# Kernel optimization log

Hardware: AMD Instinct MI355X
Metric: run time of the kernel (lower is better)

## Reference

```python
import jax, jax.numpy as jnp
import numpy as np

MARGIN = 5.0  # margin_between_clusters


def setup_inputs() -> dict:
    key = jax.random.key(0)
    k1, k2, k3 = jax.random.split(key, 3)
    N, D, K = 262144, 128, 64
    embeddings = jax.random.normal(k1, (N, D), dtype=jnp.float32)
    cluster_labels = jax.random.randint(k2, (N,), 0, K, dtype=jnp.int64)
    centroids = jax.random.normal(k3, (K, D), dtype=jnp.float32)
    return {"embeddings": embeddings, "cluster_labels": cluster_labels, "centroids": centroids}


def reference(embeddings, cluster_labels, centroids):
    # Assumes all K clusters are present in cluster_labels (true w.h.p. for N >> K),
    # matching number_cluster = len(unique(labels)) in the original.
    N, d = embeddings.shape
    K = centroids.shape[0]
    labels = cluster_labels.astype(jnp.int32)

    x2 = jnp.sum(embeddings * embeddings, axis=1, keepdims=True)        # [N,1]
    c2 = jnp.sum(centroids * centroids, axis=1)[None, :]                # [1,K]
    d2 = jnp.maximum(x2 + c2 - 2.0 * (embeddings @ centroids.T), 0.0)  # [N,K]
    dist = jnp.sqrt(d2)

    rows = jnp.arange(N)
    own_d = dist[rows, labels]                 # distance to own centroid
    counts = jax.ops.segment_sum(jnp.ones((N,), embeddings.dtype), labels, num_segments=K)
    safe_counts = jnp.maximum(counts, 1.0)

    # attraction: per cluster, mean of squared distance to own centroid
    attr_per_cluster = jax.ops.segment_sum(own_d * own_d, labels, num_segments=K) / safe_counts
    attraction_loss = jnp.sum(jnp.where(counts > 0, attr_per_cluster, 0.0))

    # repulsion: per cluster, mean over (points_in_cluster x other_centroids) of relu((m - d)^2)
    rep = jax.nn.relu((MARGIN - dist) ** 2)    # [N,K]
    row_other = (jnp.sum(rep, axis=1) - rep[rows, labels]) / (K - 1)
    rep_per_cluster = jax.ops.segment_sum(row_other, labels, num_segments=K) / safe_counts
    repulsion_loss = jnp.sum(jnp.where(counts > 0, rep_per_cluster, 0.0))

    return (attraction_loss + repulsion_loss) / K
```

## Files before the change

### kernel.cpp

```cpp
#include <hip/hip_runtime.h>


constexpr int N = 262144;
constexpr int D = 128;
constexpr int K = 64;

constexpr int GRID = 1024;
constexpr int NWAVES = 4;
constexpr int TILES_PER_WAVE = (N / 32) / (GRID * NWAVES);

typedef __bf16 bf16x8 __attribute__((ext_vector_type(8)));
typedef float  f32x16 __attribute__((ext_vector_type(16)));

__global__ __launch_bounds__(256) void dcl_main(
    const float* __restrict__ emb,
    const int*   __restrict__ labels,
    const float* __restrict__ cent,
    float* __restrict__ g_attr,
    float* __restrict__ g_rep,
    int*   __restrict__ g_cnt)
{
    __shared__ bf16x8 sA[2 * 8 * 64];
    __shared__ float  s_c2[K];
    __shared__ float  s_attr[K];
    __shared__ float  s_rep[K];
    __shared__ int    s_cnt[K];

    const int tid = threadIdx.x;

    #pragma unroll
    for (int e = tid; e < 2 * 8 * 64; e += 256) {
        const int t = e >> 9, s = (e >> 6) & 7, l = e & 63;
        const int c  = t * 32 + (l & 31);
        const int d0 = 16 * s + 8 * (l >> 5);
        const float4 f0 = *(const float4*)(cent + c * D + d0);
        const float4 f1 = *(const float4*)(cent + c * D + d0 + 4);
        bf16x8 v;
        v[0] = (__bf16)f0.x; v[1] = (__bf16)f0.y; v[2] = (__bf16)f0.z; v[3] = (__bf16)f0.w;
        v[4] = (__bf16)f1.x; v[5] = (__bf16)f1.y; v[6] = (__bf16)f1.z; v[7] = (__bf16)f1.w;
        sA[e] = v;
    }
    if (tid < K) {
        const float4* cp = (const float4*)(cent + tid * D);
        float s = 0.f;
        #pragma unroll
        for (int q = 0; q < D / 4; ++q) {
            const float4 f = cp[q];
            s = fmaf(f.x, f.x, s); s = fmaf(f.y, f.y, s);
            s = fmaf(f.z, f.z, s); s = fmaf(f.w, f.w, s);
        }
        s_c2[tid] = s;
        s_attr[tid] = 0.f; s_rep[tid] = 0.f; s_cnt[tid] = 0;
    }
    __syncthreads();

    const int wave = tid >> 6;
    const int lane = tid & 63;
    const int l31  = lane & 31;
    const int h    = lane >> 5;

    for (int tt = 0; tt < TILES_PER_WAVE; ++tt) {
        const int tile = (blockIdx.x * NWAVES + wave) * TILES_PER_WAVE + tt;
        const int p    = tile * 32 + l31;
        const int lbl  = labels[p];
        const float* xrow = emb + (size_t)p * D + 8 * h;

        f32x16 acc0 = {0.f,0.f,0.f,0.f,0.f,0.f,0.f,0.f,0.f,0.f,0.f,0.f,0.f,0.f,0.f,0.f};
        f32x16 acc1 = {0.f,0.f,0.f,0.f,0.f,0.f,0.f,0.f,0.f,0.f,0.f,0.f,0.f,0.f,0.f,0.f};
        float x2p = 0.f;

        #pragma unroll
        for (int s = 0; s < 8; ++s) {
            const float4 f0 = *(const float4*)(xrow + 16 * s);
            const float4 f1 = *(const float4*)(xrow + 16 * s + 4);
            x2p = fmaf(f0.x, f0.x, x2p); x2p = fmaf(f0.y, f0.y, x2p);
            x2p = fmaf(f0.z, f0.z, x2p); x2p = fmaf(f0.w, f0.w, x2p);
            x2p = fmaf(f1.x, f1.x, x2p); x2p = fmaf(f1.y, f1.y, x2p);
            x2p = fmaf(f1.z, f1.z, x2p); x2p = fmaf(f1.w, f1.w, x2p);
            bf16x8 b;
            b[0] = (__bf16)f0.x; b[1] = (__bf16)f0.y; b[2] = (__bf16)f0.z; b[3] = (__bf16)f0.w;
            b[4] = (__bf16)f1.x; b[5] = (__bf16)f1.y; b[6] = (__bf16)f1.z; b[7] = (__bf16)f1.w;
            const bf16x8 a0 = sA[s * 64 + lane];
            const bf16x8 a1 = sA[(8 + s) * 64 + lane];
            acc0 = __builtin_amdgcn_mfma_f32_32x32x16_bf16(a0, b, acc0, 0, 0, 0);
            acc1 = __builtin_amdgcn_mfma_f32_32x32x16_bf16(a1, b, acc1, 0, 0, 0);
        }

        const float x2 = x2p + __shfl_xor(x2p, 32);

        float s1 = 0.f, s2 = 0.f, own = 0.f;
        #pragma unroll
        for (int r = 0; r < 16; ++r) {
            const int rbase = (r & 3) + 8 * (r >> 2) + 4 * h;
            {
                const float c2r = s_c2[rbase];
                float d2 = fmaf(-2.f, acc0[r], x2 + c2r);
                d2 = fmaxf(d2, 0.f);
                const float dd = __builtin_amdgcn_sqrtf(d2);
                s1 += dd; s2 += d2;
                if (rbase == lbl) own += d2;
            }
            {
                const int row = rbase + 32;
                const float c2r = s_c2[row];
                float d2 = fmaf(-2.f, acc1[r], x2 + c2r);
                d2 = fmaxf(d2, 0.f);
                const float dd = __builtin_amdgcn_sqrtf(d2);
                s1 += dd; s2 += d2;
                if (row == lbl) own += d2;
            }
        }
        s1  += __shfl_xor(s1, 32);
        s2  += __shfl_xor(s2, 32);
        own += __shfl_xor(own, 32);

        if (lane < 32) {
            const float down = __builtin_amdgcn_sqrtf(own);
            const float own_term = fmaf(-10.f, down, 25.f) + own;
            const float row_other = (25.f * K - 10.f * s1 + s2 - own_term) * (1.f / (K - 1));
            atomicAdd(&s_attr[lbl], own);
            atomicAdd(&s_rep[lbl], row_other);
            atomicAdd(&s_cnt[lbl], 1);
        }
    }

    __syncthreads();
    if (tid < K) {
        atomicAdd(&g_attr[tid], s_attr[tid]);
        atomicAdd(&g_rep[tid], s_rep[tid]);
        atomicAdd(&g_cnt[tid], s_cnt[tid]);
    }
}

__global__ void dcl_finish(const float* __restrict__ g_attr,
                           const float* __restrict__ g_rep,
                           const int*   __restrict__ g_cnt,
                           float* __restrict__ out)
{
    const int k = threadIdx.x;
    const float cnt = (float)g_cnt[k];
    float v = (cnt > 0.f) ? (g_attr[k] + g_rep[k]) / cnt : 0.f;
    #pragma unroll
    for (int off = 32; off > 0; off >>= 1) v += __shfl_down(v, off);
    if (k == 0) out[0] = v * (1.f / K);
}

extern "C" void kernel_launch(void* const* d_in, const int* in_sizes, int n_in,
                              void* d_out, int out_size, void* d_ws, size_t ws_size,
                              hipStream_t stream) {
    const float* emb    = (const float*)d_in[0];
    const int*   labels = (const int*)d_in[1];
    const float* cent   = (const float*)d_in[2];
    float* out = (float*)d_out;

    float* g_attr = (float*)d_ws;
    float* g_rep  = g_attr + K;
    int*   g_cnt  = (int*)(g_rep + K);

    hipMemsetAsync(d_ws, 0, 3 * K * sizeof(float), stream);
    dcl_main<<<GRID, 256, 0, stream>>>(emb, labels, cent, g_attr, g_rep, g_cnt);
    dcl_finish<<<1, 64, 0, stream>>>(g_attr, g_rep, g_cnt, out);
}
```

Before: 218.3 us.

## Coalesce embedding loads, prefetch next tile, and transpose through LDS panel

Each wave now loads its whole 32x128 embedding tile with fully coalesced float4 reads into registers. It converts the tile to bf16 and writes it into a padded per-wave LDS panel, then reads MFMA B-operands back from that panel. The next tile's loads are issued before the current tile's MFMAs, and the first tile's loads are issued before the centroid setup, so global latency overlaps with compute. The row norm x2 is now computed from the bf16-rounded values, which slightly lowers precision. The change also adds 64 buffered VGPRs and extra LDS traffic.

New measurement: 207.4 us. -5.0%, faster.

```diff
diff --git a/kernel.cpp b/kernel.cpp
--- a/kernel.cpp
+++ b/kernel.cpp
@@ -7,8 +7,10 @@
 
 constexpr int GRID = 1024;
 constexpr int NWAVES = 4;
-constexpr int TILES_PER_WAVE = (N / 32) / (GRID * NWAVES);
+constexpr int TPW = (N / 32) / (GRID * NWAVES);
+constexpr int PANEL = 34 * 32;
 
+typedef __bf16 bf16x4 __attribute__((ext_vector_type(4)));
 typedef __bf16 bf16x8 __attribute__((ext_vector_type(8)));
 typedef float  f32x16 __attribute__((ext_vector_type(16)));
 
@@ -21,12 +23,26 @@
     int*   __restrict__ g_cnt)
 {
     __shared__ bf16x8 sA[2 * 8 * 64];
+    __shared__ __align__(16) bf16x4 sPanel[NWAVES * PANEL];
     __shared__ float  s_c2[K];
     __shared__ float  s_attr[K];
     __shared__ float  s_rep[K];
     __shared__ int    s_cnt[K];
 
-    const int tid = threadIdx.x;
+    const int tid  = threadIdx.x;
+    const int wave = tid >> 6;
+    const int lane = tid & 63;
+    const int l31  = lane & 31;
+    const int h    = lane >> 5;
+
+    const int tile0 = (blockIdx.x * NWAVES + wave) * TPW;
+
+    float4 buf[16];
+    {
+        const float4* src = (const float4*)emb + (size_t)tile0 * 1024 + lane;
+        #pragma unroll
+        for (int q = 0; q < 16; ++q) buf[q] = src[q * 64];
+    }
 
     #pragma unroll
     for (int e = tid; e < 2 * 8 * 64; e += 256) {
@@ -54,16 +70,26 @@
     }
     __syncthreads();
 
-    const int wave = tid >> 6;
-    const int lane = tid & 63;
-    const int l31  = lane & 31;
-    const int h    = lane >> 5;
+    bf16x4* panel = sPanel + wave * PANEL;
 
-    for (int tt = 0; tt < TILES_PER_WAVE; ++tt) {
-        const int tile = (blockIdx.x * NWAVES + wave) * TILES_PER_WAVE + tt;
-        const int p    = tile * 32 + l31;
-        const int lbl  = labels[p];
-        const float* xrow = emb + (size_t)p * D + 8 * h;
+    for (int tt = 0; tt < TPW; ++tt) {
+        const int tile = tile0 + tt;
+        const int lbl  = labels[tile * 32 + l31];
+
+        #pragma unroll
+        for (int q = 0; q < 16; ++q) {
+            bf16x4 v;
+            v[0] = (__bf16)buf[q].x; v[1] = (__bf16)buf[q].y;
+            v[2] = (__bf16)buf[q].z; v[3] = (__bf16)buf[q].w;
+            const int n = 2 * q + h;
+            panel[34 * n + l31] = v;
+        }
+
+        if (tt + 1 < TPW) {
+            const float4* src = (const float4*)emb + (size_t)(tile + 1) * 1024 + lane;
+            #pragma unroll
+            for (int q = 0; q < 16; ++q) buf[q] = src[q * 64];
+        }
 
         f32x16 acc0 = {0.f,0.f,0.f,0.f,0.f,0.f,0.f,0.f,0.f,0.f,0.f,0.f,0.f,0.f,0.f,0.f};
         f32x16 acc1 = {0.f,0.f,0.f,0.f,0.f,0.f,0.f,0.f,0.f,0.f,0.f,0.f,0.f,0.f,0.f,0.f};
@@ -71,15 +97,12 @@
 
         #pragma unroll
         for (int s = 0; s < 8; ++s) {
-            const float4 f0 = *(const float4*)(xrow + 16 * s);
-            const float4 f1 = *(const float4*)(xrow + 16 * s + 4);
-            x2p = fmaf(f0.x, f0.x, x2p); x2p = fmaf(f0.y, f0.y, x2p);
-            x2p = fmaf(f0.z, f0.z, x2p); x2p = fmaf(f0.w, f0.w, x2p);
-            x2p = fmaf(f1.x, f1.x, x2p); x2p = fmaf(f1.y, f1.y, x2p);
-            x2p = fmaf(f1.z, f1.z, x2p); x2p = fmaf(f1.w, f1.w, x2p);
-            bf16x8 b;
-            b[0] = (__bf16)f0.x; b[1] = (__bf16)f0.y; b[2] = (__bf16)f0.z; b[3] = (__bf16)f0.w;
-            b[4] = (__bf16)f1.x; b[5] = (__bf16)f1.y; b[6] = (__bf16)f1.z; b[7] = (__bf16)f1.w;
+            const bf16x8 b = *(const bf16x8*)&panel[34 * l31 + 4 * s + 2 * h];
+            #pragma unroll
+            for (int e = 0; e < 8; ++e) {
+                const float fe = (float)b[e];
+                x2p = fmaf(fe, fe, x2p);
+            }
             const bf16x8 a0 = sA[s * 64 + lane];
             const bf16x8 a1 = sA[(8 + s) * 64 + lane];
             acc0 = __builtin_amdgcn_mfma_f32_32x32x16_bf16(a0, b, acc0, 0, 0, 0);
```
